# Kernel tuning notes

Measured on AMD Instinct MI355X. Metric: run time of the kernel, lower is better.

The kernel has to match this reference:

```python
import jax, jax.numpy as jnp
import numpy as np

H = 16      # num_heads
D = 64      # hidden_size per head
IN = 1024   # input_size = H*D
B, S = 4, 2048

def setup_inputs() -> dict:
    key = jax.random.key(0)
    ks = jax.random.split(key, 5)
    scale = 1.0 / np.sqrt(IN)
    return {
        "x": jax.random.normal(ks[0], (B, S, IN), dtype=jnp.float32),
        "Wq": jax.random.normal(ks[1], (IN, H * D), dtype=jnp.float32) * scale,
        "bq": jnp.zeros((H * D,), dtype=jnp.float32),
        "Wk": jax.random.normal(ks[2], (IN, H * D), dtype=jnp.float32) * scale,
        "bk": jnp.zeros((H * D,), dtype=jnp.float32),
        "Wv": jax.random.normal(ks[3], (IN, H * D), dtype=jnp.float32) * scale,
        "bv": jnp.zeros((H * D,), dtype=jnp.float32),
        "Wo": jax.random.normal(ks[4], (H * D, IN), dtype=jnp.float32) * scale,
        "bo": jnp.zeros((IN,), dtype=jnp.float32),
    }

def reference(x, Wq, bq, Wk, bk, Wv, bv, Wo, bo):
    b, s, _ = x.shape
    # projections -> [b, h, s, d]
    def split_heads(t):
        return t.reshape(b, s, H, D).transpose(0, 2, 1, 3)
    q = split_heads(x @ Wq + bq)
    k = split_heads(x @ Wk + bk)
    v = split_heads(x @ Wv + bv)
    scores = jnp.einsum('bhqd,bhkd->bhqk', q, k) / jnp.sqrt(jnp.float32(D))
    probs = jax.nn.softmax(scores, axis=-1)            # [b,h,s,s]
    attn = jnp.einsum('bhqk,bhkd->bhqd', probs, v)     # [b,h,s,d]
    attn = attn.transpose(0, 2, 1, 3).reshape(b, s, H * D)
    out = attn @ Wo + bo
    return out, jnp.mean(probs, axis=1)
```

## Files before the change

kernel.cpp:

```cpp
#include <hip/hip_runtime.h>

typedef __attribute__((ext_vector_type(8))) short s8v;
typedef __attribute__((ext_vector_type(4))) short s4v;
typedef __attribute__((ext_vector_type(4))) float f4v;

#define DEV __device__ __forceinline__

DEV short b16(float f) {
  unsigned u = __builtin_bit_cast(unsigned, f);
  u = (u + 0x7fffu + ((u >> 16) & 1u)) >> 16;
  return (short)u;
}

DEV unsigned pk2(float a, float b) {
#if __has_builtin(__builtin_amdgcn_cvt_pk_bf16_f32)
  auto p = __builtin_amdgcn_cvt_pk_bf16_f32(a, b);
  return __builtin_bit_cast(unsigned, p);
#else
  return (unsigned)(unsigned short)b16(a) | ((unsigned)(unsigned short)b16(b) << 16);
#endif
}

DEV float fexp2(float x) {
#if __has_builtin(__builtin_amdgcn_exp2f)
  return __builtin_amdgcn_exp2f(x);
#else
  return exp2f(x);
#endif
}

DEV void gl_lds16(const short* g, short* l) {
  __builtin_amdgcn_global_load_lds((const __attribute__((address_space(1))) void*)g,
                                   (__attribute__((address_space(3))) void*)l, 16, 0, 0);
}

#define WAIT_VM(N) asm volatile("s_waitcnt vmcnt(" #N ")" ::: "memory")
#define WAIT_LGKM0() asm volatile("s_waitcnt lgkmcnt(0)" ::: "memory")
#define BAR() __builtin_amdgcn_s_barrier()

__global__ __launch_bounds__(256) void cast_f32_bf16(const float* __restrict__ in,
                                                     short* __restrict__ out, int n4) {
  int i = blockIdx.x * 256 + threadIdx.x;
  if (i >= n4) return;
  float4 v = ((const float4*)in)[i];
  s4v o; o.x = b16(v.x); o.y = b16(v.y); o.z = b16(v.z); o.w = b16(v.w);
  ((s4v*)out)[i] = o;
}

__global__ __launch_bounds__(256) void wtrans4(const float* __restrict__ W0, const float* __restrict__ W1,
                                               const float* __restrict__ W2, const float* __restrict__ W3,
                                               short* __restrict__ Wt) {
  const int mat = blockIdx.y;
  const float* W = mat == 0 ? W0 : (mat == 1 ? W1 : (mat == 2 ? W2 : W3));
  short* out = Wt + (long)mat * 1048576;
  int id = blockIdx.x * 256 + threadIdx.x;
  int k8 = id >> 10;
  int n  = id & 1023;
  s8v o;
#pragma unroll
  for (int j = 0; j < 8; ++j) o[j] = b16(W[(k8 * 8 + j) * 1024 + n]);
  *(s8v*)&out[n * 1024 + k8 * 8] = o;
}

__global__ __launch_bounds__(256) void gemm_qkv(const short* __restrict__ A,
                                                const short* __restrict__ Wt,
                                                const float* __restrict__ bq,
                                                const float* __restrict__ bk,
                                                const float* __restrict__ bv,
                                                short* __restrict__ Cb, float qscale) {
  __shared__ short As[128 * 64];
  __shared__ short Bs[128 * 64];
  int n = blockIdx.x + 24 * blockIdx.y;
  int id = (n & 7) * 192 + (n >> 3);
  const int nx = id % 24, my = id / 24;
  const int mat = nx >> 3;
  const short* Bt = Wt + (long)mat * 1048576;
  const float* bias = mat == 0 ? bq : (mat == 1 ? bk : bv);
  short* Cout = Cb + (long)mat * 8388608;
  const float scale = mat == 0 ? qscale : 1.0f;
  const int m0 = my * 128, n0 = (nx & 7) * 128;
  const int tid = threadIdx.x;
  const int w = tid >> 6, lane = tid & 63, quad = lane >> 4, l15 = lane & 15;
  const int wm = w >> 1, wn = w & 1;
  const int lr = lane >> 3, lc = (lane & 7) * 8;
  f4v acc[4][4] = {};
  for (int k0 = 0; k0 < 1024; k0 += 64) {
#pragma unroll
    for (int i = 0; i < 4; ++i) {
      int c = i * 4 + w;
      int r = c * 8 + lr;
      gl_lds16(&A[(m0 + r) * 1024 + k0 + lc], &As[c * 512]);
      gl_lds16(&Bt[(n0 + r) * 1024 + k0 + lc], &Bs[c * 512]);
    }
    __syncthreads();
#pragma unroll
    for (int kk = 0; kk < 2; ++kk) {
      s8v af[4], bf[4];
#pragma unroll
      for (int mt = 0; mt < 4; ++mt) af[mt] = *(const s8v*)&As[(wm * 64 + mt * 16 + l15) * 64 + kk * 32 + quad * 8];
#pragma unroll
      for (int nt = 0; nt < 4; ++nt) bf[nt] = *(const s8v*)&Bs[(wn * 64 + nt * 16 + l15) * 64 + kk * 32 + quad * 8];
#pragma unroll
      for (int mt = 0; mt < 4; ++mt)
#pragma unroll
        for (int nt = 0; nt < 4; ++nt)
          acc[mt][nt] = __builtin_amdgcn_mfma_f32_16x16x32_bf16(af[mt], bf[nt], acc[mt][nt], 0, 0, 0);
    }
    __syncthreads();
  }
#pragma unroll
  for (int nt = 0; nt < 4; ++nt) {
    const int col = n0 + wn * 64 + nt * 16 + l15;
    const float bcol = bias[col];
#pragma unroll
    for (int mt = 0; mt < 4; ++mt)
#pragma unroll
      for (int r = 0; r < 4; ++r) {
        const int row = m0 + wm * 64 + mt * 16 + quad * 4 + r;
        Cout[row * 1024 + col] = b16((acc[mt][nt][r] + bcol) * scale);
      }
  }
}

__global__ __launch_bounds__(256) void gemm128(const short* __restrict__ A,
                                               const short* __restrict__ Bt,
                                               const float* __restrict__ bias,
                                               float* __restrict__ Cout) {
  __shared__ short As[128 * 64];
  __shared__ short Bs[128 * 64];
  int n = blockIdx.x + 8 * blockIdx.y;
  int id = (n & 7) * 64 + (n >> 3);
  const int m0 = (id >> 3) * 128, n0 = (id & 7) * 128;
  const int tid = threadIdx.x;
  const int w = tid >> 6, lane = tid & 63, quad = lane >> 4, l15 = lane & 15;
  const int wm = w >> 1, wn = w & 1;
  const int lr = lane >> 3, lc = (lane & 7) * 8;
  f4v acc[4][4] = {};
  for (int k0 = 0; k0 < 1024; k0 += 64) {
#pragma unroll
    for (int i = 0; i < 4; ++i) {
      int c = i * 4 + w;
      int r = c * 8 + lr;
      gl_lds16(&A[(m0 + r) * 1024 + k0 + lc], &As[c * 512]);
      gl_lds16(&Bt[(n0 + r) * 1024 + k0 + lc], &Bs[c * 512]);
    }
    __syncthreads();
#pragma unroll
    for (int kk = 0; kk < 2; ++kk) {
      s8v af[4], bf[4];
#pragma unroll
      for (int mt = 0; mt < 4; ++mt) af[mt] = *(const s8v*)&As[(wm * 64 + mt * 16 + l15) * 64 + kk * 32 + quad * 8];
#pragma unroll
      for (int nt = 0; nt < 4; ++nt) bf[nt] = *(const s8v*)&Bs[(wn * 64 + nt * 16 + l15) * 64 + kk * 32 + quad * 8];
#pragma unroll
      for (int mt = 0; mt < 4; ++mt)
#pragma unroll
        for (int nt = 0; nt < 4; ++nt)
          acc[mt][nt] = __builtin_amdgcn_mfma_f32_16x16x32_bf16(af[mt], bf[nt], acc[mt][nt], 0, 0, 0);
    }
    __syncthreads();
  }
#pragma unroll
  for (int nt = 0; nt < 4; ++nt) {
    const int col = n0 + wn * 64 + nt * 16 + l15;
    const float bcol = bias[col];
#pragma unroll
    for (int mt = 0; mt < 4; ++mt)
#pragma unroll
      for (int r = 0; r < 4; ++r) {
        const int row = m0 + wm * 64 + mt * 16 + quad * 4 + r;
        Cout[row * 1024 + col] = acc[mt][nt][r] + bcol;
      }
  }
}

__global__ __launch_bounds__(256) void vtrans(const short* __restrict__ V, short* __restrict__ Vt) {
  __shared__ short T[128][72];
  const int st = blockIdx.x, h = blockIdx.y, b = blockIdx.z;
  const int tid = threadIdx.x;
#pragma unroll
  for (int i = 0; i < 4; ++i) {
    int c = tid + i * 256;
    int r = c >> 3, c8 = (c & 7) * 8;
    *(s8v*)&T[r][c8] = *(const s8v*)&V[((b * 2048 + st * 128 + r) * 16 + h) * 64 + c8];
  }
  __syncthreads();
#pragma unroll
  for (int i = 0; i < 4; ++i) {
    int id = tid + i * 256;
    int d = id & 63, s8 = id >> 6;
    s8v o;
#pragma unroll
    for (int j = 0; j < 8; ++j) o[j] = T[s8 * 8 + j][d];
    *(s8v*)&Vt[((b * 16 + h) * 64 + d) * 2048 + st * 128 + s8 * 8] = o;
  }
}

__global__ __launch_bounds__(256, 3) void attn_ctx(const short* __restrict__ Q, const short* __restrict__ K,
                                                   const short* __restrict__ Vt,
                                                   float* __restrict__ rbuf, short* __restrict__ ctx) {
  __shared__ __align__(16) char smem[49152];
  short* Ks = (short*)smem;
  short* Vs = (short*)(smem + 16384);
  short* Ps = (short*)(smem + 32768);
  short* Qs = Ps;
  int nlin = blockIdx.x + 32 * (blockIdx.y + 16 * blockIdx.z);
  int bid = (nlin & 7) * 256 + (nlin >> 3);
  const int q64 = bid & 31, h = (bid >> 5) & 15, b = bid >> 9;
  const int tid = threadIdx.x, w = tid >> 6, lane = tid & 63, quad = lane >> 4, l15 = lane & 15;
  const int bh = b * 16 + h, q0 = q64 * 64;

#pragma unroll
  for (int i = 0; i < 2; ++i) {
    int c = tid + i * 256;
    int r = c >> 3, cc = c & 7;
    *(s8v*)&Qs[r * 64 + (((cc ^ (r & 7))) << 3)] =
        *(const s8v*)&Q[((b * 2048 + q0 + r) * 16 + h) * 64 + cc * 8];
  }
  __syncthreads();
  s8v qf[4][2];
#pragma unroll
  for (int nt = 0; nt < 4; ++nt) {
    int r = nt * 16 + l15;
    qf[nt][0] = *(const s8v*)&Qs[r * 64 + ((quad ^ (r & 7)) << 3)];
    qf[nt][1] = *(const s8v*)&Qs[r * 64 + (((4 + quad) ^ (r & 7)) << 3)];
  }
  const short* kbase = &K[((long)(b * 2048) * 16 + h) * 64];
  const short* vbase = &Vt[(long)(bh * 64) * 2048];
  const int krow = w * 8 + (lane >> 3);
  const short* ksrc = kbase + krow * 1024 + (((lane & 7) ^ (lane >> 3)) << 3);
  const int vrow = w * 4 + (lane >> 4);
  const short* vsrc = vbase + vrow * 2048 + (((lane & 15) ^ vrow) << 3);
  f4v o[4] = {};
  f4v lf = {};
  s8v ones;
#pragma unroll
  for (int j = 0; j < 8; ++j) ones[j] = (short)0x3F80;

#pragma unroll
  for (int i = 0; i < 4; ++i) gl_lds16(ksrc + i * 32768, &Ks[(i * 4 + w) * 512]);
#pragma unroll
  for (int i = 0; i < 4; ++i) gl_lds16(vsrc + i * 32768, &Vs[(i * 4 + w) * 512]);
  WAIT_LGKM0();

  for (int kt = 0; kt < 16; ++kt) {
    WAIT_VM(4);
    BAR();
#pragma unroll
    for (int mt = 0; mt < 2; ++mt) {
      int kr = w * 32 + mt * 16 + l15;
      s8v a0 = *(const s8v*)&Ks[kr * 64 + ((quad ^ (kr & 7)) << 3)];
      s8v a1 = *(const s8v*)&Ks[kr * 64 + (((4 + quad) ^ (kr & 7)) << 3)];
#pragma unroll
      for (int nt = 0; nt < 4; ++nt) {
        f4v st = {};
        st = __builtin_amdgcn_mfma_f32_16x16x32_bf16(a0, qf[nt][0], st, 0, 0, 0);
        st = __builtin_amdgcn_mfma_f32_16x16x32_bf16(a1, qf[nt][1], st, 0, 0, 0);
        float e0 = fexp2(st[0]), e1 = fexp2(st[1]);
        float e2 = fexp2(st[2]), e3 = fexp2(st[3]);
        uint2 pp; pp.x = pk2(e0, e1); pp.y = pk2(e2, e3);
        int q = nt * 16 + l15;
        int chunk = (w * 4 + mt * 2 + (quad >> 1)) ^ l15;
        *(uint2*)&Ps[q * 128 + (chunk << 3) + (quad & 1) * 4] = pp;
      }
    }
    WAIT_LGKM0();
    BAR();
    if (kt < 15) {
#pragma unroll
      for (int i = 0; i < 4; ++i) gl_lds16(ksrc + (kt + 1) * 131072 + i * 32768, &Ks[(i * 4 + w) * 512]);
      WAIT_VM(4);
    } else {
      WAIT_VM(0);
    }
    BAR();
#pragma unroll
    for (int kk = 0; kk < 4; ++kk) {
      int qr = w * 16 + l15;
      s8v a = *(const s8v*)&Ps[qr * 128 + (((kk * 4 + quad) ^ (qr & 15)) << 3)];
#pragma unroll
      for (int dt = 0; dt < 4; ++dt) {
        int d = dt * 16 + l15;
        s8v vb = *(const s8v*)&Vs[d * 128 + (((kk * 4 + quad) ^ (d & 15)) << 3)];
        o[dt] = __builtin_amdgcn_mfma_f32_16x16x32_bf16(a, vb, o[dt], 0, 0, 0);
      }
      lf = __builtin_amdgcn_mfma_f32_16x16x32_bf16(a, ones, lf, 0, 0, 0);
    }
    WAIT_LGKM0();
    BAR();
    if (kt < 15) {
#pragma unroll
      for (int i = 0; i < 4; ++i) gl_lds16(vsrc + (kt + 1) * 128 + i * 32768, &Vs[(i * 4 + w) * 512]);
    }
  }

  float rv[4];
#pragma unroll
  for (int r = 0; r < 4; ++r) rv[r] = 1.0f / lf[r];
  if (l15 == 0) {
    f4v t; t[0] = rv[0]; t[1] = rv[1]; t[2] = rv[2]; t[3] = rv[3];
    *(f4v*)&rbuf[bh * 2048 + q0 + w * 16 + quad * 4] = t;
  }
#pragma unroll
  for (int dt = 0; dt < 4; ++dt)
#pragma unroll
    for (int r = 0; r < 4; ++r) {
      int sq = q0 + w * 16 + quad * 4 + r;
      ctx[((b * 2048 + sq) * 16 + h) * 64 + dt * 16 + l15] = b16(o[dt][r] * rv[r]);
    }
}

__global__ __launch_bounds__(256) void mean_probs(const short* __restrict__ Q, const short* __restrict__ K,
                                                  const float* __restrict__ rbuf, float* __restrict__ outm) {
  __shared__ __align__(16) short Qs[2][8192];
  __shared__ __align__(16) short Ks[2][8192];
  __shared__ __align__(16) float r_all[2048];
  int nlin = blockIdx.x + 16 * (blockIdx.y + 16 * blockIdx.z);
  int bid = (nlin & 7) * 128 + (nlin >> 3);
  const int k128 = bid & 15, q128 = (bid >> 4) & 15, b = bid >> 8;
  const int tid = threadIdx.x, w = tid >> 6, lane = tid & 63, quad = lane >> 4, l15 = lane & 15;
  f4v mn[2][8] = {};
  const int mrow = w * 8 + (lane >> 3);
  const int mck8 = ((lane & 7) ^ (lane >> 3)) << 3;
  const short* qsrc = Q + ((long)(b * 2048 + q128 * 128 + mrow) * 16) * 64 + mck8;
  const short* ksrc = K + ((long)(b * 2048 + k128 * 128 + mrow) * 16) * 64 + mck8;
  const float* rb = rbuf + (long)(b * 16) * 2048 + q128 * 128;
#pragma unroll
  for (int i = 0; i < 2; ++i) {
    int hh = i * 8 + w * 2 + (lane >> 5);
    gl_lds16((const short*)(rb + hh * 2048 + (lane & 31) * 4), (short*)r_all + (i * 4 + w) * 512);
  }
#pragma unroll
  for (int i = 0; i < 4; ++i) gl_lds16(qsrc + i * 32768, &Qs[0][(i * 4 + w) * 512]);
#pragma unroll
  for (int i = 0; i < 4; ++i) gl_lds16(ksrc + i * 32768, &Ks[0][(i * 4 + w) * 512]);

  for (int h = 0; h < 16; ++h) {
    const int cur = h & 1;
    if (h < 15) {
#pragma unroll
      for (int i = 0; i < 4; ++i) gl_lds16(qsrc + (h + 1) * 64 + i * 32768, &Qs[cur ^ 1][(i * 4 + w) * 512]);
#pragma unroll
      for (int i = 0; i < 4; ++i) gl_lds16(ksrc + (h + 1) * 64 + i * 32768, &Ks[cur ^ 1][(i * 4 + w) * 512]);
      WAIT_VM(8);
    } else {
      WAIT_VM(0);
    }
    BAR();
    s8v aq[2][2];
#pragma unroll
    for (int qt = 0; qt < 2; ++qt) {
      int r = w * 32 + qt * 16 + l15;
      aq[qt][0] = *(const s8v*)&Qs[cur][r * 64 + ((quad ^ (r & 7)) << 3)];
      aq[qt][1] = *(const s8v*)&Qs[cur][r * 64 + (((4 + quad) ^ (r & 7)) << 3)];
    }
    float rr[2][4];
#pragma unroll
    for (int qt = 0; qt < 2; ++qt)
#pragma unroll
      for (int r = 0; r < 4; ++r) rr[qt][r] = r_all[h * 128 + w * 32 + qt * 16 + quad * 4 + r];
#pragma unroll
    for (int ktile = 0; ktile < 8; ++ktile) {
      int kr = ktile * 16 + l15;
      s8v b0 = *(const s8v*)&Ks[cur][kr * 64 + ((quad ^ (kr & 7)) << 3)];
      s8v b1 = *(const s8v*)&Ks[cur][kr * 64 + (((4 + quad) ^ (kr & 7)) << 3)];
#pragma unroll
      for (int qt = 0; qt < 2; ++qt) {
        f4v sc = {};
        sc = __builtin_amdgcn_mfma_f32_16x16x32_bf16(aq[qt][0], b0, sc, 0, 0, 0);
        sc = __builtin_amdgcn_mfma_f32_16x16x32_bf16(aq[qt][1], b1, sc, 0, 0, 0);
#pragma unroll
        for (int r = 0; r < 4; ++r)
          mn[qt][ktile][r] += fexp2(sc[r]) * rr[qt][r];
      }
    }
    WAIT_LGKM0();
    BAR();
  }
#pragma unroll
  for (int qt = 0; qt < 2; ++qt)
#pragma unroll
    for (int ktile = 0; ktile < 8; ++ktile)
#pragma unroll
      for (int r = 0; r < 4; ++r) {
        long qrow = q128 * 128 + w * 32 + qt * 16 + quad * 4 + r;
        outm[((long)b * 2048 + qrow) * 2048 + k128 * 128 + ktile * 16 + l15] = mn[qt][ktile][r] * 0.0625f;
      }
}

extern "C" void kernel_launch(void* const* d_in, const int* in_sizes, int n_in,
                              void* d_out, int out_size, void* d_ws, size_t ws_size,
                              hipStream_t stream) {
  (void)in_sizes; (void)n_in; (void)out_size; (void)ws_size;
  const float* x  = (const float*)d_in[0];
  const float* Wq = (const float*)d_in[1];
  const float* bq = (const float*)d_in[2];
  const float* Wk = (const float*)d_in[3];
  const float* bk = (const float*)d_in[4];
  const float* Wv = (const float*)d_in[5];
  const float* bv = (const float*)d_in[6];
  const float* Wo = (const float*)d_in[7];
  const float* bo = (const float*)d_in[8];
  float* out  = (float*)d_out;
  float* outm = out + 8388608;

  char* ws = (char*)d_ws;
  short* xb  = (short*)(ws);
  short* Wqt = (short*)(ws + 16777216);
  short* Wot = (short*)(ws + 23068672);
  short* Qb  = (short*)(ws + 25165824);
  short* Kb  = (short*)(ws + 41943040);
  short* Vb  = (short*)(ws + 58720256);
  short* Vt  = (short*)(ws + 75497472);
  float* rbuf = (float*)Vb;
  short* ctx = xb;

  const float C2 = 0.18033688011112042f;

  cast_f32_bf16<<<8192, 256, 0, stream>>>(x, xb, 2097152);
  wtrans4<<<dim3(512, 4), 256, 0, stream>>>(Wq, Wk, Wv, Wo, Wqt);
  gemm_qkv<<<dim3(24, 64), 256, 0, stream>>>(xb, Wqt, bq, bk, bv, Qb, C2);
  vtrans<<<dim3(16, 16, 4), 256, 0, stream>>>(Vb, Vt);
  attn_ctx<<<dim3(32, 16, 4), 256, 0, stream>>>(Qb, Kb, Vt, rbuf, ctx);
  mean_probs<<<dim3(16, 16, 4), 256, 0, stream>>>(Qb, Kb, rbuf, outm);
  gemm128<<<dim3(8, 64), 256, 0, stream>>>(ctx, Wot, bo, out);
}
```

Before: 413.2 us.

## Fuse V transpose into QKV GEMM epilogue and double-buffer attention K/V tiles

New measurement: 425.7 us. +3.0%, slower.

```diff
diff --git a/kernel.cpp b/kernel.cpp
--- a/kernel.cpp
+++ b/kernel.cpp
@@ -67,7 +67,8 @@
                                                 const float* __restrict__ bq,
                                                 const float* __restrict__ bk,
                                                 const float* __restrict__ bv,
-                                                short* __restrict__ Cb, float qscale) {
+                                                short* __restrict__ Cb,
+                                                short* __restrict__ Vt, float qscale) {
   __shared__ short As[128 * 64];
   __shared__ short Bs[128 * 64];
   int n = blockIdx.x + 24 * blockIdx.y;
@@ -108,17 +109,34 @@
     }
     __syncthreads();
   }
-#pragma unroll
-  for (int nt = 0; nt < 4; ++nt) {
-    const int col = n0 + wn * 64 + nt * 16 + l15;
-    const float bcol = bias[col];
-#pragma unroll
-    for (int mt = 0; mt < 4; ++mt)
-#pragma unroll
-      for (int r = 0; r < 4; ++r) {
-        const int row = m0 + wm * 64 + mt * 16 + quad * 4 + r;
-        Cout[row * 1024 + col] = b16((acc[mt][nt][r] + bcol) * scale);
+  if (mat == 2) {
+#pragma unroll
+    for (int nt = 0; nt < 4; ++nt) {
+      const int col = n0 + wn * 64 + nt * 16 + l15;
+      const float bcol = bias[col];
+      const long cbase = ((long)(col >> 6)) * 64 + (col & 63);
+#pragma unroll
+      for (int mt = 0; mt < 4; ++mt) {
+        const int row0 = m0 + wm * 64 + mt * 16 + quad * 4;
+        s4v pv;
+#pragma unroll
+        for (int r = 0; r < 4; ++r) pv[r] = b16(acc[mt][nt][r] + bcol);
+        *(s4v*)&Vt[(((long)(row0 >> 11) * 1024) + cbase) * 2048 + (row0 & 2047)] = pv;
       }
+    }
+  } else {
+#pragma unroll
+    for (int nt = 0; nt < 4; ++nt) {
+      const int col = n0 + wn * 64 + nt * 16 + l15;
+      const float bcol = bias[col];
+#pragma unroll
+      for (int mt = 0; mt < 4; ++mt)
+#pragma unroll
+        for (int r = 0; r < 4; ++r) {
+          const int row = m0 + wm * 64 + mt * 16 + quad * 4 + r;
+          Cout[row * 1024 + col] = b16((acc[mt][nt][r] + bcol) * scale);
+        }
+    }
   }
 }
 
@@ -174,123 +192,92 @@
   }
 }
 
-__global__ __launch_bounds__(256) void vtrans(const short* __restrict__ V, short* __restrict__ Vt) {
-  __shared__ short T[128][72];
-  const int st = blockIdx.x, h = blockIdx.y, b = blockIdx.z;
-  const int tid = threadIdx.x;
-#pragma unroll
-  for (int i = 0; i < 4; ++i) {
-    int c = tid + i * 256;
-    int r = c >> 3, c8 = (c & 7) * 8;
-    *(s8v*)&T[r][c8] = *(const s8v*)&V[((b * 2048 + st * 128 + r) * 16 + h) * 64 + c8];
-  }
-  __syncthreads();
-#pragma unroll
-  for (int i = 0; i < 4; ++i) {
-    int id = tid + i * 256;
-    int d = id & 63, s8 = id >> 6;
-    s8v o;
-#pragma unroll
-    for (int j = 0; j < 8; ++j) o[j] = T[s8 * 8 + j][d];
-    *(s8v*)&Vt[((b * 16 + h) * 64 + d) * 2048 + st * 128 + s8 * 8] = o;
-  }
-}
-
-__global__ __launch_bounds__(256, 3) void attn_ctx(const short* __restrict__ Q, const short* __restrict__ K,
+__global__ __launch_bounds__(256, 4) void attn_ctx(const short* __restrict__ Q, const short* __restrict__ K,
                                                    const short* __restrict__ Vt,
                                                    float* __restrict__ rbuf, short* __restrict__ ctx) {
-  __shared__ __align__(16) char smem[49152];
-  short* Ks = (short*)smem;
-  short* Vs = (short*)(smem + 16384);
-  short* Ps = (short*)(smem + 32768);
-  short* Qs = Ps;
+  __shared__ __align__(16) char smem[40960];
   int nlin = blockIdx.x + 32 * (blockIdx.y + 16 * blockIdx.z);
   int bid = (nlin & 7) * 256 + (nlin >> 3);
   const int q64 = bid & 31, h = (bid >> 5) & 15, b = bid >> 9;
   const int tid = threadIdx.x, w = tid >> 6, lane = tid & 63, quad = lane >> 4, l15 = lane & 15;
   const int bh = b * 16 + h, q0 = q64 * 64;
+  short* Qs = (short*)(smem + 32768);
+  short* Ps = Qs;
+
+  const short* kbase = &K[((long)(b * 2048) * 16 + h) * 64];
+  const short* vbase = &Vt[(long)(bh * 64) * 2048];
+  const int lr3 = lane >> 3;
+  const int lc3 = ((lane & 7) ^ lr3) << 3;
+  const short* ksrc = kbase + (w * 8 + lr3) * 1024 + lc3;
+  const short* vsrc = vbase + (w * 8 + lr3) * 2048 + lc3;
+
+  gl_lds16(ksrc,          (short*)smem + w * 512);
+  gl_lds16(ksrc + 32768,  (short*)smem + (4 + w) * 512);
+  gl_lds16(vsrc,          (short*)(smem + 16384) + w * 512);
+  gl_lds16(vsrc + 65536,  (short*)(smem + 16384) + (4 + w) * 512);
 
 #pragma unroll
   for (int i = 0; i < 2; ++i) {
     int c = tid + i * 256;
     int r = c >> 3, cc = c & 7;
-    *(s8v*)&Qs[r * 64 + (((cc ^ (r & 7))) << 3)] =
+    *(s8v*)&Qs[r * 64 + ((cc ^ (r & 7)) << 3)] =
         *(const s8v*)&Q[((b * 2048 + q0 + r) * 16 + h) * 64 + cc * 8];
   }
   __syncthreads();
-  s8v qf[4][2];
-#pragma unroll
-  for (int nt = 0; nt < 4; ++nt) {
-    int r = nt * 16 + l15;
-    qf[nt][0] = *(const s8v*)&Qs[r * 64 + ((quad ^ (r & 7)) << 3)];
-    qf[nt][1] = *(const s8v*)&Qs[r * 64 + (((4 + quad) ^ (r & 7)) << 3)];
-  }
-  const short* kbase = &K[((long)(b * 2048) * 16 + h) * 64];
-  const short* vbase = &Vt[(long)(bh * 64) * 2048];
-  const int krow = w * 8 + (lane >> 3);
-  const short* ksrc = kbase + krow * 1024 + (((lane & 7) ^ (lane >> 3)) << 3);
-  const int vrow = w * 4 + (lane >> 4);
-  const short* vsrc = vbase + vrow * 2048 + (((lane & 15) ^ vrow) << 3);
+  const int qrow = w * 16 + l15;
+  s8v qb0 = *(const s8v*)&Qs[qrow * 64 + ((quad ^ (qrow & 7)) << 3)];
+  s8v qb1 = *(const s8v*)&Qs[qrow * 64 + (((4 + quad) ^ (qrow & 7)) << 3)];
+  WAIT_LGKM0();
+  __builtin_amdgcn_sched_barrier(0);
+
   f4v o[4] = {};
   f4v lf = {};
   s8v ones;
 #pragma unroll
   for (int j = 0; j < 8; ++j) ones[j] = (short)0x3F80;
 
-#pragma unroll
-  for (int i = 0; i < 4; ++i) gl_lds16(ksrc + i * 32768, &Ks[(i * 4 + w) * 512]);
-#pragma unroll
-  for (int i = 0; i < 4; ++i) gl_lds16(vsrc + i * 32768, &Vs[(i * 4 + w) * 512]);
-  WAIT_LGKM0();
-
-  for (int kt = 0; kt < 16; ++kt) {
-    WAIT_VM(4);
+  for (int kt = 0; kt < 32; ++kt) {
+    const int cur = kt & 1;
+    short* KsC = (short*)(smem + cur * 8192);
+    short* VsC = (short*)(smem + 16384 + cur * 8192);
+    WAIT_VM(0);
     BAR();
-#pragma unroll
-    for (int mt = 0; mt < 2; ++mt) {
-      int kr = w * 32 + mt * 16 + l15;
-      s8v a0 = *(const s8v*)&Ks[kr * 64 + ((quad ^ (kr & 7)) << 3)];
-      s8v a1 = *(const s8v*)&Ks[kr * 64 + (((4 + quad) ^ (kr & 7)) << 3)];
-#pragma unroll
-      for (int nt = 0; nt < 4; ++nt) {
-        f4v st = {};
-        st = __builtin_amdgcn_mfma_f32_16x16x32_bf16(a0, qf[nt][0], st, 0, 0, 0);
-        st = __builtin_amdgcn_mfma_f32_16x16x32_bf16(a1, qf[nt][1], st, 0, 0, 0);
-        float e0 = fexp2(st[0]), e1 = fexp2(st[1]);
-        float e2 = fexp2(st[2]), e3 = fexp2(st[3]);
-        uint2 pp; pp.x = pk2(e0, e1); pp.y = pk2(e2, e3);
-        int q = nt * 16 + l15;
-        int chunk = (w * 4 + mt * 2 + (quad >> 1)) ^ l15;
-        *(uint2*)&Ps[q * 128 + (chunk << 3) + (quad & 1) * 4] = pp;
-      }
+    if (kt < 31) {
+      short* KsN = (short*)(smem + (cur ^ 1) * 8192);
+      short* VsN = (short*)(smem + 16384 + (cur ^ 1) * 8192);
+      const short* kp = ksrc + (kt + 1) * 65536;
+      const short* vp = vsrc + (kt + 1) * 64;
+      gl_lds16(kp,          KsN + w * 512);
+      gl_lds16(kp + 32768,  KsN + (4 + w) * 512);
+      gl_lds16(vp,          VsN + w * 512);
+      gl_lds16(vp + 65536,  VsN + (4 + w) * 512);
+    }
+#pragma unroll
+    for (int ktile = 0; ktile < 4; ++ktile) {
+      int kr = ktile * 16 + l15;
+      s8v a0 = *(const s8v*)&KsC[kr * 64 + ((quad ^ (kr & 7)) << 3)];
+      s8v a1 = *(const s8v*)&KsC[kr * 64 + (((4 + quad) ^ (kr & 7)) << 3)];
+      f4v st = {};
+      st = __builtin_amdgcn_mfma_f32_16x16x32_bf16(a0, qb0, st, 0, 0, 0);
+      st = __builtin_amdgcn_mfma_f32_16x16x32_bf16(a1, qb1, st, 0, 0, 0);
+      float e0 = fexp2(st[0]), e1 = fexp2(st[1]);
+      float e2 = fexp2(st[2]), e3 = fexp2(st[3]);
+      uint2 pp; pp.x = pk2(e0, e1); pp.y = pk2(e2, e3);
+      int chunk = (ktile * 2 + (quad >> 1)) ^ (l15 & 7);
+      *(uint2*)&Ps[qrow * 64 + (chunk << 3) + (quad & 1) * 4] = pp;
     }
     WAIT_LGKM0();
-    BAR();
-    if (kt < 15) {
-#pragma unroll
-      for (int i = 0; i < 4; ++i) gl_lds16(ksrc + (kt + 1) * 131072 + i * 32768, &Ks[(i * 4 + w) * 512]);
-      WAIT_VM(4);
-    } else {
-      WAIT_VM(0);
-    }
-    BAR();
-#pragma unroll
-    for (int kk = 0; kk < 4; ++kk) {
-      int qr = w * 16 + l15;
-      s8v a = *(const s8v*)&Ps[qr * 128 + (((kk * 4 + quad) ^ (qr & 15)) << 3)];
+    __builtin_amdgcn_sched_barrier(0);
+#pragma unroll
+    for (int kk = 0; kk < 2; ++kk) {
+      s8v a = *(const s8v*)&Ps[qrow * 64 + (((kk * 4 + quad) ^ (l15 & 7)) << 3)];
 #pragma unroll
       for (int dt = 0; dt < 4; ++dt) {
         int d = dt * 16 + l15;
-        s8v vb = *(const s8v*)&Vs[d * 128 + (((kk * 4 + quad) ^ (d & 15)) << 3)];
+        s8v vb = *(const s8v*)&VsC[d * 64 + (((kk * 4 + quad) ^ (d & 7)) << 3)];
         o[dt] = __builtin_amdgcn_mfma_f32_16x16x32_bf16(a, vb, o[dt], 0, 0, 0);
       }
       lf = __builtin_amdgcn_mfma_f32_16x16x32_bf16(a, ones, lf, 0, 0, 0);
-    }
-    WAIT_LGKM0();
-    BAR();
-    if (kt < 15) {
-#pragma unroll
-      for (int i = 0; i < 4; ++i) gl_lds16(vsrc + (kt + 1) * 128 + i * 32768, &Vs[(i * 4 + w) * 512]);
     }
   }
 
@@ -337,16 +324,14 @@
 
   for (int h = 0; h < 16; ++h) {
     const int cur = h & 1;
+    WAIT_VM(0);
+    BAR();
     if (h < 15) {
 #pragma unroll
       for (int i = 0; i < 4; ++i) gl_lds16(qsrc + (h + 1) * 64 + i * 32768, &Qs[cur ^ 1][(i * 4 + w) * 512]);
 #pragma unroll
       for (int i = 0; i < 4; ++i) gl_lds16(ksrc + (h + 1) * 64 + i * 32768, &Ks[cur ^ 1][(i * 4 + w) * 512]);
-      WAIT_VM(8);
-    } else {
-      WAIT_VM(0);
-    }
-    BAR();
+    }
     s8v aq[2][2];
 #pragma unroll
     for (int qt = 0; qt < 2; ++qt) {
@@ -374,8 +359,6 @@
           mn[qt][ktile][r] += fexp2(sc[r]) * rr[qt][r];
       }
     }
-    WAIT_LGKM0();
-    BAR();
   }
 #pragma unroll
   for (int qt = 0; qt < 2; ++qt)
@@ -410,17 +393,15 @@
   short* Wot = (short*)(ws + 23068672);
   short* Qb  = (short*)(ws + 25165824);
   short* Kb  = (short*)(ws + 41943040);
-  short* Vb  = (short*)(ws + 58720256);
   short* Vt  = (short*)(ws + 75497472);
-  float* rbuf = (float*)Vb;
+  float* rbuf = (float*)(ws + 58720256);
   short* ctx = xb;
 
   const float C2 = 0.18033688011112042f;
 
   cast_f32_bf16<<<8192, 256, 0, stream>>>(x, xb, 2097152);
   wtrans4<<<dim3(512, 4), 256, 0, stream>>>(Wq, Wk, Wv, Wo, Wqt);
-  gemm_qkv<<<dim3(24, 64), 256, 0, stream>>>(xb, Wqt, bq, bk, bv, Qb, C2);
-  vtrans<<<dim3(16, 16, 4), 256, 0, stream>>>(Vb, Vt);
+  gemm_qkv<<<dim3(24, 64), 256, 0, stream>>>(xb, Wqt, bq, bk, bv, Qb, Vt, C2);
   attn_ctx<<<dim3(32, 16, 4), 256, 0, stream>>>(Qb, Kb, Vt, rbuf, ctx);
   mean_probs<<<dim3(16, 16, 4), 256, 0, stream>>>(Qb, Kb, rbuf, outm);
   gemm128<<<dim3(8, 64), 256, 0, stream>>>(ctx, Wot, bo, out);
```

## Fuse V transpose into QKV GEMM epilogue and restructure mean_probs sync

Applied to the files above, without the earlier changes.

New measurement: 414.3 us. Within noise of the previous version (+0.3%).

```diff
diff --git a/kernel.cpp b/kernel.cpp
--- a/kernel.cpp
+++ b/kernel.cpp
@@ -67,9 +67,11 @@
                                                 const float* __restrict__ bq,
                                                 const float* __restrict__ bk,
                                                 const float* __restrict__ bv,
-                                                short* __restrict__ Cb, float qscale) {
-  __shared__ short As[128 * 64];
-  __shared__ short Bs[128 * 64];
+                                                short* __restrict__ Cb,
+                                                short* __restrict__ Vt, float qscale) {
+  __shared__ short AB[16384];
+  short* As = AB;
+  short* Bs = AB + 8192;
   int n = blockIdx.x + 24 * blockIdx.y;
   int id = (n & 7) * 192 + (n >> 3);
   const int nx = id % 24, my = id / 24;
@@ -108,17 +110,44 @@
     }
     __syncthreads();
   }
-#pragma unroll
-  for (int nt = 0; nt < 4; ++nt) {
-    const int col = n0 + wn * 64 + nt * 16 + l15;
-    const float bcol = bias[col];
-#pragma unroll
-    for (int mt = 0; mt < 4; ++mt)
-#pragma unroll
-      for (int r = 0; r < 4; ++r) {
-        const int row = m0 + wm * 64 + mt * 16 + quad * 4 + r;
-        Cout[row * 1024 + col] = b16((acc[mt][nt][r] + bcol) * scale);
-      }
+  if (mat == 2) {
+    short* T = AB;
+#pragma unroll
+    for (int nt = 0; nt < 4; ++nt) {
+      const int c = wn * 64 + nt * 16 + l15;
+      const float bcol = bias[n0 + c];
+#pragma unroll
+      for (int mt = 0; mt < 4; ++mt) {
+        const int sr = wm * 64 + mt * 16 + quad * 4;
+#pragma unroll
+        for (int r = 0; r < 4; ++r) {
+          int s = sr + r;
+          T[c * 128 + ((((s >> 3) ^ (c & 15))) << 3) + (s & 7)] = b16(acc[mt][nt][r] + bcol);
+        }
+      }
+    }
+    __syncthreads();
+    const int b = m0 >> 11, s0 = m0 & 2047, h0 = n0 >> 6;
+#pragma unroll
+    for (int i = 0; i < 8; ++i) {
+      int unit = tid + i * 256;
+      int c = unit >> 4, s8 = unit & 15;
+      s8v v = *(const s8v*)&T[c * 128 + ((s8 ^ (c & 15)) << 3)];
+      *(s8v*)&Vt[(((long)(b * 16 + h0 + (c >> 6)) * 64) + (c & 63)) * 2048 + s0 + s8 * 8] = v;
+    }
+  } else {
+#pragma unroll
+    for (int nt = 0; nt < 4; ++nt) {
+      const int col = n0 + wn * 64 + nt * 16 + l15;
+      const float bcol = bias[col];
+#pragma unroll
+      for (int mt = 0; mt < 4; ++mt)
+#pragma unroll
+        for (int r = 0; r < 4; ++r) {
+          const int row = m0 + wm * 64 + mt * 16 + quad * 4 + r;
+          Cout[row * 1024 + col] = b16((acc[mt][nt][r] + bcol) * scale);
+        }
+    }
   }
 }
 
@@ -174,28 +203,6 @@
   }
 }
 
-__global__ __launch_bounds__(256) void vtrans(const short* __restrict__ V, short* __restrict__ Vt) {
-  __shared__ short T[128][72];
-  const int st = blockIdx.x, h = blockIdx.y, b = blockIdx.z;
-  const int tid = threadIdx.x;
-#pragma unroll
-  for (int i = 0; i < 4; ++i) {
-    int c = tid + i * 256;
-    int r = c >> 3, c8 = (c & 7) * 8;
-    *(s8v*)&T[r][c8] = *(const s8v*)&V[((b * 2048 + st * 128 + r) * 16 + h) * 64 + c8];
-  }
-  __syncthreads();
-#pragma unroll
-  for (int i = 0; i < 4; ++i) {
-    int id = tid + i * 256;
-    int d = id & 63, s8 = id >> 6;
-    s8v o;
-#pragma unroll
-    for (int j = 0; j < 8; ++j) o[j] = T[s8 * 8 + j][d];
-    *(s8v*)&Vt[((b * 16 + h) * 64 + d) * 2048 + st * 128 + s8 * 8] = o;
-  }
-}
-
 __global__ __launch_bounds__(256, 3) void attn_ctx(const short* __restrict__ Q, const short* __restrict__ K,
                                                    const short* __restrict__ Vt,
                                                    float* __restrict__ rbuf, short* __restrict__ ctx) {
@@ -337,16 +344,14 @@
 
   for (int h = 0; h < 16; ++h) {
     const int cur = h & 1;
+    WAIT_VM(0);
+    BAR();
     if (h < 15) {
 #pragma unroll
       for (int i = 0; i < 4; ++i) gl_lds16(qsrc + (h + 1) * 64 + i * 32768, &Qs[cur ^ 1][(i * 4 + w) * 512]);
 #pragma unroll
       for (int i = 0; i < 4; ++i) gl_lds16(ksrc + (h + 1) * 64 + i * 32768, &Ks[cur ^ 1][(i * 4 + w) * 512]);
-      WAIT_VM(8);
-    } else {
-      WAIT_VM(0);
-    }
-    BAR();
+    }
     s8v aq[2][2];
 #pragma unroll
     for (int qt = 0; qt < 2; ++qt) {
@@ -374,8 +379,6 @@
           mn[qt][ktile][r] += fexp2(sc[r]) * rr[qt][r];
       }
     }
-    WAIT_LGKM0();
-    BAR();
   }
 #pragma unroll
   for (int qt = 0; qt < 2; ++qt)
@@ -410,17 +413,15 @@
   short* Wot = (short*)(ws + 23068672);
   short* Qb  = (short*)(ws + 25165824);
   short* Kb  = (short*)(ws + 41943040);
-  short* Vb  = (short*)(ws + 58720256);
   short* Vt  = (short*)(ws + 75497472);
-  float* rbuf = (float*)Vb;
+  float* rbuf = (float*)(ws + 58720256);
   short* ctx = xb;
 
   const float C2 = 0.18033688011112042f;
 
   cast_f32_bf16<<<8192, 256, 0, stream>>>(x, xb, 2097152);
   wtrans4<<<dim3(512, 4), 256, 0, stream>>>(Wq, Wk, Wv, Wo, Wqt);
-  gemm_qkv<<<dim3(24, 64), 256, 0, stream>>>(xb, Wqt, bq, bk, bv, Qb, C2);
-  vtrans<<<dim3(16, 16, 4), 256, 0, stream>>>(Vb, Vt);
+  gemm_qkv<<<dim3(24, 64), 256, 0, stream>>>(xb, Wqt, bq, bk, bv, Qb, Vt, C2);
   attn_ctx<<<dim3(32, 16, 4), 256, 0, stream>>>(Qb, Kb, Vt, rbuf, ctx);
   mean_probs<<<dim3(16, 16, 4), 256, 0, stream>>>(Qb, Kb, rbuf, outm);
   gemm128<<<dim3(8, 64), 256, 0, stream>>>(ctx, Wot, bo, out);
```
